# Kernel tuning notes

Measured on AMD Instinct MI355X. Metric: run time of the kernel, lower is better.

Reference implementation:

```python
import jax, jax.numpy as jnp
import numpy as np

# Dims: B batch, T target seq, S source seq (self-attn: S==T), V symmetry-rep dim (D4 -> 8),
# M heads-per-group, K groups (num_heads = M*K = 8), F head_rep dim (TrivialRep -> 1),
# Hqk qk head width, Hv v head width, C feature width per rep component.
B, T, S, V, M, K, F, Hqk, Hv, C = 4, 512, 512, 8, 2, 4, 1, 32, 32, 256


def setup_inputs() -> dict:
    key = jax.random.key(0)
    ks = jax.random.split(key, 6)
    x = jax.random.normal(ks[0], (B, T, V, C), jnp.float32)
    # SymDecompLinear kernels: q has extra out reps (F, M, K); k/v have (F, 1, K) -> m axis broadcast
    Wq = jax.random.normal(ks[1], (C, M, K, F, Hqk), jnp.float32) / np.sqrt(C).astype(np.float32)
    Wk = jax.random.normal(ks[2], (C, K, F, Hqk), jnp.float32) / np.sqrt(C).astype(np.float32)
    Wv = jax.random.normal(ks[3], (C, K, F, Hv), jnp.float32) / np.sqrt(C).astype(np.float32)
    # out projection contracts the (M, K, F, Hv) head structure back to C features
    Wout = jax.random.normal(ks[4], (M, K, F, Hv, C), jnp.float32) / np.sqrt(M * K * F * Hv).astype(np.float32)
    mask = jax.random.bernoulli(ks[5], 0.9, (B, T, S))
    mask = mask.at[..., 0].set(True)  # guarantee each query attends to >=1 key
    return dict(x=x, Wq=Wq, Wk=Wk, Wv=Wv, Wout=Wout, mask=mask)


def reference(x, Wq, Wk, Wv, Wout, mask):
    # projections: q -> [B,T,V,M,K,F,Hqk]; k,v -> [B,S,V,K,F,H] (single head per group, broadcast over m)
    q = jnp.einsum('btvc,cmkfh->btvmkfh', x, Wq)
    k = jnp.einsum('bsvc,ckfh->bsvkfh', x, Wk)
    v = jnp.einsum('bsvc,ckfh->bsvkfh', x, Wv)
    scale = 1.0 / np.sqrt(F * Hqk).astype(np.float32)
    # logits retain the symmetry axis v: [B,T,S,V,M,K]
    logits = scale * jnp.einsum('btvmkfh,bsvkfh->btsvmk', q, k)
    lgmsk = mask[..., :, :, None, None, None]  # [B,T,S,1,1,1]
    weight = jax.nn.softmax(logits, axis=-4, where=lgmsk)  # softmax over source axis s
    att = jnp.einsum('btsvmk,bsvkfh->btvmkfh', weight, v)
    out = jnp.einsum('btvmkfh,mkfhc->btvc', att, Wout)
    return out
```

## Files before the change

kernel.cpp:

```cpp
#include <hip/hip_runtime.h>
#include <hip/hip_bf16.h>
#include <cstdint>

#define BB 4
#define TT 512
#define SS 512
#define VV 8
#define NROWS (BB * TT * VV)

typedef __attribute__((ext_vector_type(8))) short bf16x8;
typedef __attribute__((ext_vector_type(4))) float f32x4;

static __device__ __forceinline__ short f2bf(float f) {
  union { float f; unsigned u; } x; x.f = f;
  unsigned r = x.u + 0x7FFFu + ((x.u >> 16) & 1u);
  return (short)(r >> 16);
}

static __device__ __forceinline__ unsigned cvt_pk(float lo, float hi) {
  unsigned r;
  asm("v_cvt_pk_bf16_f32 %0, %1, %2" : "=v"(r) : "v"(lo), "v"(hi));
  return r;
}

__global__ __launch_bounds__(256) void pack_w_kernel(const float* __restrict__ Wq,
                                                     const float* __restrict__ Wk,
                                                     const float* __restrict__ Wv,
                                                     const float* __restrict__ Wout,
                                                     short* __restrict__ WcatT,
                                                     short* __restrict__ WoutT) {
  int idx = blockIdx.x * 256 + threadIdx.x;
  const float qscale = 0.17677669529663687f * 1.4426950408889634f;
  if (idx < 512 * 256) {
    int n = idx >> 8, c = idx & 255;
    float val;
    if (n < 256)      val = Wq[c * 256 + n] * qscale;
    else if (n < 384) val = Wk[c * 128 + (n - 256)];
    else              val = Wv[c * 128 + (n - 384)];
    WcatT[idx] = f2bf(val);
  } else {
    int j = idx - 512 * 256;
    int cc = j >> 8, jj = j & 255;
    WoutT[j] = f2bf(Wout[jj * 256 + cc]);
  }
}

__global__ __launch_bounds__(256) void pack_mask_kernel(const int* __restrict__ mask,
                                                        unsigned long long* __restrict__ mask64) {
  int row = blockIdx.x * 4 + (threadIdx.x >> 6);
  int ln = threadIdx.x & 63;
  const int* mrow = mask + (size_t)row * SS;
#pragma unroll
  for (int c = 0; c < 8; ++c) {
    unsigned long long bal = __ballot(mrow[c * 64 + ln] != 0);
    if (ln == 0) mask64[(size_t)row * 8 + c] = bal;
  }
}

__global__ __launch_bounds__(256) void vtrans_kernel(const short* __restrict__ qkv,
                                                     short* __restrict__ Vt) {
  const int sc = blockIdx.x;
  const int v = blockIdx.y, b = blockIdx.z;
  const int k = threadIdx.x & 3;
  const int sp = threadIdx.x >> 2;
  const int s = sc * 128 + sp * 2;
  const short* src0 = qkv + ((size_t)((b * TT + s) * VV + v)) * 512 + 384 + k * 32;
  const short* src1 = src0 + VV * 512;
  bf16x8 r0[4], r1[4];
#pragma unroll
  for (int i = 0; i < 4; ++i) {
    r0[i] = *(const bf16x8*)(src0 + i * 8);
    r1[i] = *(const bf16x8*)(src1 + i * 8);
  }
  short* dst = Vt + ((size_t)((b * VV + v) * 4 + k)) * 32 * 512 + s;
#pragma unroll
  for (int h = 0; h < 32; ++h) {
    unsigned pk = (unsigned)(unsigned short)r0[h >> 3][h & 7] |
                  ((unsigned)(unsigned short)r1[h >> 3][h & 7] << 16);
    *(unsigned*)(dst + (size_t)h * 512) = pk;
  }
}

template <int N, bool AF32, bool OUTF32>
__global__ __launch_bounds__(256) void gemm_bf16(const void* __restrict__ Ap,
                                                 const short* __restrict__ Bt,
                                                 void* __restrict__ Cout) {
  __shared__ short As[128][64];
  __shared__ short Bs[128][64];
  const int tid = threadIdx.x;
  const int w = tid >> 6, ln = tid & 63;
  const int wr = (w >> 1) * 64, wc = (w & 1) * 64;
  const int bm = blockIdx.x * 128, bn = blockIdx.y * 128;
  const int lr = ln & 15, lk = (ln >> 4) * 8;
  const int r0 = tid >> 3, ko = (tid & 7) * 8;

  f32x4 acc[4][4] = {};

  for (int k0 = 0; k0 < 256; k0 += 64) {
    bf16x8 a[4], bb[4];
#pragma unroll
    for (int i = 0; i < 4; ++i) {
      size_t row = (size_t)(bm + i * 32 + r0);
      if constexpr (AF32) {
        const float* Af = (const float*)Ap;
        float4 f0 = *(const float4*)&Af[row * 256 + k0 + ko];
        float4 f1 = *(const float4*)&Af[row * 256 + k0 + ko + 4];
        uint4 pk = make_uint4(cvt_pk(f0.x, f0.y), cvt_pk(f0.z, f0.w),
                              cvt_pk(f1.x, f1.y), cvt_pk(f1.z, f1.w));
        a[i] = *(bf16x8*)&pk;
      } else {
        a[i] = *(const bf16x8*)&((const short*)Ap)[row * 256 + k0 + ko];
      }
      bb[i] = *(const bf16x8*)&Bt[(size_t)(bn + i * 32 + r0) * 256 + k0 + ko];
    }
    __syncthreads();
#pragma unroll
    for (int i = 0; i < 4; ++i) {
      *(bf16x8*)&As[i * 32 + r0][ko] = a[i];
      *(bf16x8*)&Bs[i * 32 + r0][ko] = bb[i];
    }
    __syncthreads();

#pragma unroll
    for (int kk = 0; kk < 2; ++kk) {
      bf16x8 af[4], bfr[4];
#pragma unroll
      for (int mi = 0; mi < 4; ++mi)
        af[mi] = *(const bf16x8*)&As[wr + mi * 16 + lr][kk * 32 + lk];
#pragma unroll
      for (int ni = 0; ni < 4; ++ni)
        bfr[ni] = *(const bf16x8*)&Bs[wc + ni * 16 + lr][kk * 32 + lk];
#pragma unroll
      for (int mi = 0; mi < 4; ++mi)
#pragma unroll
        for (int ni = 0; ni < 4; ++ni)
          acc[mi][ni] = __builtin_amdgcn_mfma_f32_16x16x32_bf16(af[mi], bfr[ni], acc[mi][ni], 0, 0, 0);
    }
  }

  const int rowg = (ln >> 4) * 4;
#pragma unroll
  for (int mi = 0; mi < 4; ++mi)
#pragma unroll
    for (int r = 0; r < 4; ++r) {
      size_t row = bm + wr + mi * 16 + rowg + r;
      if constexpr (OUTF32) {
#pragma unroll
        for (int ni = 0; ni < 4; ++ni)
          ((float*)Cout)[row * N + bn + wc + ni * 16 + lr] = acc[mi][ni][r];
      } else {
        unsigned u0 = cvt_pk(acc[mi][0][r], acc[mi][1][r]);
        unsigned u1 = cvt_pk(acc[mi][2][r], acc[mi][3][r]);
        short* Cs = (short*)Cout + row * N + bn + wc + lr;
        Cs[0]  = (short)u0;
        Cs[16] = (short)(u0 >> 16);
        Cs[32] = (short)u1;
        Cs[48] = (short)(u1 >> 16);
      }
    }
}

__global__ __launch_bounds__(256) void attn_mfma(const short* __restrict__ qkv,
                                                 const short* __restrict__ Vt,
                                                 const unsigned long long* __restrict__ mask64,
                                                 short* __restrict__ att) {
  const int t0 = blockIdx.x * 64;
  const int v  = blockIdx.y >> 2;
  const int k  = blockIdx.y & 3;
  const int b  = blockIdx.z;
  const int tid = threadIdx.x;
  const int w  = tid >> 6;
  const int ln = tid & 63;
  const int gq = ln >> 4;
  const int tr = ln & 15;

  __shared__ __align__(16) short Pt[4][16][72];

  bf16x8 qf[2];
  {
    const short* qp = qkv + ((size_t)((b*TT + t0 + w*16 + tr)*VV + v))*512 + k*32 + gq*8;
    qf[0] = *(const bf16x8*)qp;
    qf[1] = *(const bf16x8*)(qp + 128);
  }

  f32x4 acc_o[2][2] = {};
  float l_run[2] = {0.f, 0.f};

  const short* kbase = qkv + ((size_t)(b*TT*VV + v))*512 + 256 + k*32 + gq*8;
  const short* vbase = Vt + ((size_t)((b*VV + v)*4 + k))*32*512 + (size_t)tr*512 + gq*8;
  const unsigned long long* mrow = mask64 + ((size_t)(b*TT + t0 + w*16 + tr))*8;

  bf16x8 kf[4], vf[2][2];
  unsigned long long mb;
#pragma unroll
  for (int st = 0; st < 4; ++st)
    kf[st] = *(const bf16x8*)(kbase + (size_t)(st*16 + tr) * (VV*512));
#pragma unroll
  for (int sh = 0; sh < 2; ++sh)
#pragma unroll
    for (int hh = 0; hh < 2; ++hh)
      vf[sh][hh] = *(const bf16x8*)(vbase + hh*16*512 + sh*32);
  mb = mrow[0];

  for (int c = 0; c < 8; ++c) {
    bf16x8 kn[4], vn[2][2];
    unsigned long long mbn;
    if (c < 7) {
      const int sb = (c + 1) * 64;
#pragma unroll
      for (int st = 0; st < 4; ++st)
        kn[st] = *(const bf16x8*)(kbase + (size_t)(sb + st*16 + tr) * (VV*512));
#pragma unroll
      for (int sh = 0; sh < 2; ++sh)
#pragma unroll
        for (int hh = 0; hh < 2; ++hh)
          vn[sh][hh] = *(const bf16x8*)(vbase + hh*16*512 + sb + sh*32);
      mbn = mrow[c + 1];
    }

    unsigned mlo = (unsigned)mb, mhi = (unsigned)(mb >> 32);
    float bias[4][4];
#pragma unroll
    for (int st = 0; st < 4; ++st) {
      unsigned wbits = (st < 2) ? mlo : mhi;
      const int base = (st & 1) * 16 + 4 * gq;
#pragma unroll
      for (int r = 0; r < 4; ++r)
        bias[st][r] = ((wbits >> (base + r)) & 1u) ? 0.f : -INFINITY;
    }

#pragma unroll
    for (int m = 0; m < 2; ++m) {
      f32x4 lac[4];
#pragma unroll
      for (int st = 0; st < 4; ++st) {
        f32x4 z = {0.f, 0.f, 0.f, 0.f};
        lac[st] = __builtin_amdgcn_mfma_f32_16x16x32_bf16(kf[st], qf[m], z, 0, 0, 0);
      }
      float pl[4][4];
      float rs = 0.f;
#pragma unroll
      for (int st = 0; st < 4; ++st)
#pragma unroll
        for (int r = 0; r < 4; ++r) {
          pl[st][r] = exp2f(lac[st][r] + bias[st][r]);
          rs += pl[st][r];
        }
      rs += __shfl_xor(rs, 16);
      rs += __shfl_xor(rs, 32);
      l_run[m] += rs;

#pragma unroll
      for (int st = 0; st < 4; ++st)
        *(uint2*)&Pt[w][tr][st * 16 + 4 * gq] =
            make_uint2(cvt_pk(pl[st][0], pl[st][1]), cvt_pk(pl[st][2], pl[st][3]));
#pragma unroll
      for (int sh = 0; sh < 2; ++sh) {
        bf16x8 pf = *(const bf16x8*)&Pt[w][tr][sh * 32 + gq * 8];
#pragma unroll
        for (int hh = 0; hh < 2; ++hh)
          acc_o[m][hh] = __builtin_amdgcn_mfma_f32_16x16x32_bf16(pf, vf[sh][hh], acc_o[m][hh], 0, 0, 0);
      }
    }

    if (c < 7) {
#pragma unroll
      for (int st = 0; st < 4; ++st) kf[st] = kn[st];
#pragma unroll
      for (int sh = 0; sh < 2; ++sh)
#pragma unroll
        for (int hh = 0; hh < 2; ++hh) vf[sh][hh] = vn[sh][hh];
      mb = mbn;
    }
  }

#pragma unroll
  for (int m = 0; m < 2; ++m) {
    float invR[4];
#pragma unroll
    for (int r = 0; r < 4; ++r) invR[r] = 1.f / __shfl(l_run[m], 4 * gq + r);
#pragma unroll
    for (int r = 0; r < 4; ++r) {
      short* dst = att + ((size_t)((b*TT + t0 + w*16 + 4*gq + r)*VV + v))*256
                 + m*128 + k*32 + tr;
      unsigned u = cvt_pk(acc_o[m][0][r] * invR[r], acc_o[m][1][r] * invR[r]);
      dst[0]  = (short)u;
      dst[16] = (short)(u >> 16);
    }
  }
}

extern "C" void kernel_launch(void* const* d_in, const int* in_sizes, int n_in,
                              void* d_out, int out_size, void* d_ws, size_t ws_size,
                              hipStream_t stream) {
  const float* x = (const float*)d_in[0];
  const float* Wq = (const float*)d_in[1];
  const float* Wk = (const float*)d_in[2];
  const float* Wv = (const float*)d_in[3];
  const float* Wout = (const float*)d_in[4];
  const int* mask = (const int*)d_in[5];
  float* out = (float*)d_out;

  short* WcatT = (short*)d_ws;
  short* WoutT = WcatT + 512 * 256;
  short* qkv   = WoutT + 256 * 256;
  short* att   = qkv + (size_t)NROWS * 512;
  short* Vt    = att + (size_t)NROWS * 256;
  unsigned long long* mask64 = (unsigned long long*)(Vt + (size_t)128 * 32 * 512);

  pack_w_kernel<<<(512 * 256 + 256 * 256) / 256, 256, 0, stream>>>(Wq, Wk, Wv, Wout, WcatT, WoutT);
  pack_mask_kernel<<<BB * TT / 4, 256, 0, stream>>>(mask, mask64);
  gemm_bf16<512, true, false><<<dim3(NROWS / 128, 4), 256, 0, stream>>>(x, WcatT, qkv);
  vtrans_kernel<<<dim3(4, VV, BB), 256, 0, stream>>>(qkv, Vt);
  attn_mfma<<<dim3(TT / 64, VV * 4, BB), 256, 0, stream>>>(qkv, Vt, mask64, att);
  gemm_bf16<256, false, true><<<dim3(NROWS / 128, 2), 256, 0, stream>>>(att, WoutT, out);
}
```

Before: 75.22 us.

## Store QKV head-major and tile V transpose; merge weight and mask packing kernels

The QKV GEMM epilogue now writes its output in a per-(batch, view, head) contiguous layout, [bv][head][t][32]. K loads in the attention kernel therefore become contiguous 64-byte rows instead of strided by V*512. The V transpose is rewritten to read this layout and to write V^T in 64-column tiles, and the weight packing and mask packing kernels are merged into a single launch. The goal is better memory coalescing in attention and one less kernel launch. In exchange, the GEMM epilogue now does scattered 2-byte stores with more index arithmetic.

Result: faster. 68.55 us (-8.9%).

```diff
diff --git a/kernel.cpp b/kernel.cpp
--- a/kernel.cpp
+++ b/kernel.cpp
@@ -8,6 +8,7 @@
 #define VV 8
 #define NROWS (BB * TT * VV)
 
+
 typedef __attribute__((ext_vector_type(8))) short bf16x8;
 typedef __attribute__((ext_vector_type(4))) float f32x4;
 
@@ -23,65 +24,63 @@
   return r;
 }
 
-__global__ __launch_bounds__(256) void pack_w_kernel(const float* __restrict__ Wq,
-                                                     const float* __restrict__ Wk,
-                                                     const float* __restrict__ Wv,
-                                                     const float* __restrict__ Wout,
-                                                     short* __restrict__ WcatT,
-                                                     short* __restrict__ WoutT) {
-  int idx = blockIdx.x * 256 + threadIdx.x;
-  const float qscale = 0.17677669529663687f * 1.4426950408889634f;
-  if (idx < 512 * 256) {
-    int n = idx >> 8, c = idx & 255;
-    float val;
-    if (n < 256)      val = Wq[c * 256 + n] * qscale;
-    else if (n < 384) val = Wk[c * 128 + (n - 256)];
-    else              val = Wv[c * 128 + (n - 384)];
-    WcatT[idx] = f2bf(val);
+__global__ __launch_bounds__(256) void pack_all_kernel(const float* __restrict__ Wq,
+                                                       const float* __restrict__ Wk,
+                                                       const float* __restrict__ Wv,
+                                                       const float* __restrict__ Wout,
+                                                       const int* __restrict__ mask,
+                                                       short* __restrict__ WcatT,
+                                                       short* __restrict__ WoutT,
+                                                       unsigned long long* __restrict__ mask64) {
+  if (blockIdx.x < 768) {
+    int idx = blockIdx.x * 256 + threadIdx.x;
+    const float qscale = 0.17677669529663687f * 1.4426950408889634f;
+    if (idx < 512 * 256) {
+      int n = idx >> 8, c = idx & 255;
+      float val;
+      if (n < 256)      val = Wq[c * 256 + n] * qscale;
+      else if (n < 384) val = Wk[c * 128 + (n - 256)];
+      else              val = Wv[c * 128 + (n - 384)];
+      WcatT[idx] = f2bf(val);
+    } else {
+      int j = idx - 512 * 256;
+      int cc = j >> 8, jj = j & 255;
+      WoutT[j] = f2bf(Wout[jj * 256 + cc]);
+    }
   } else {
-    int j = idx - 512 * 256;
-    int cc = j >> 8, jj = j & 255;
-    WoutT[j] = f2bf(Wout[jj * 256 + cc]);
-  }
-}
-
-__global__ __launch_bounds__(256) void pack_mask_kernel(const int* __restrict__ mask,
-                                                        unsigned long long* __restrict__ mask64) {
-  int row = blockIdx.x * 4 + (threadIdx.x >> 6);
-  int ln = threadIdx.x & 63;
-  const int* mrow = mask + (size_t)row * SS;
-#pragma unroll
-  for (int c = 0; c < 8; ++c) {
-    unsigned long long bal = __ballot(mrow[c * 64 + ln] != 0);
-    if (ln == 0) mask64[(size_t)row * 8 + c] = bal;
-  }
-}
-
-__global__ __launch_bounds__(256) void vtrans_kernel(const short* __restrict__ qkv,
-                                                     short* __restrict__ Vt) {
-  const int sc = blockIdx.x;
-  const int v = blockIdx.y, b = blockIdx.z;
-  const int k = threadIdx.x & 3;
-  const int sp = threadIdx.x >> 2;
-  const int s = sc * 128 + sp * 2;
-  const short* src0 = qkv + ((size_t)((b * TT + s) * VV + v)) * 512 + 384 + k * 32;
-  const short* src1 = src0 + VV * 512;
+    int row = (blockIdx.x - 768) * 4 + (threadIdx.x >> 6);
+    int ln = threadIdx.x & 63;
+    const int* mrow = mask + (size_t)row * SS;
+#pragma unroll
+    for (int c = 0; c < 8; ++c) {
+      unsigned long long bal = __ballot(mrow[c * 64 + ln] != 0);
+      if (ln == 0) mask64[(size_t)row * 8 + c] = bal;
+    }
+  }
+}
+
+__global__ __launch_bounds__(256) void vtrans_kernel(const short* __restrict__ qkvh,
+                                                     short* __restrict__ Vt2) {
+  const int hd = blockIdx.x;
+  const int bv = hd >> 2, k = hd & 3;
+  const int s0 = threadIdx.x * 2;
+  const short* src = qkvh + ((size_t)(bv * 16 + 12 + k) * 512 + s0) * 32;
   bf16x8 r0[4], r1[4];
 #pragma unroll
   for (int i = 0; i < 4; ++i) {
-    r0[i] = *(const bf16x8*)(src0 + i * 8);
-    r1[i] = *(const bf16x8*)(src1 + i * 8);
-  }
-  short* dst = Vt + ((size_t)((b * VV + v) * 4 + k)) * 32 * 512 + s;
+    r0[i] = *(const bf16x8*)(src + i * 8);
+    r1[i] = *(const bf16x8*)(src + 32 + i * 8);
+  }
+  short* dst = Vt2 + (size_t)hd * 16384 + (s0 >> 6) * 2048 + (s0 & 63);
 #pragma unroll
   for (int h = 0; h < 32; ++h) {
     unsigned pk = (unsigned)(unsigned short)r0[h >> 3][h & 7] |
                   ((unsigned)(unsigned short)r1[h >> 3][h & 7] << 16);
-    *(unsigned*)(dst + (size_t)h * 512) = pk;
-  }
-}
-
-template <int N, bool AF32, bool OUTF32>
+    *(unsigned*)(dst + h * 64) = pk;
+  }
+}
+
+template <int N, bool AF32, int EPI>
 __global__ __launch_bounds__(256) void gemm_bf16(const void* __restrict__ Ap,
                                                  const short* __restrict__ Bt,
                                                  void* __restrict__ Cout) {
@@ -139,29 +138,44 @@
   }
 
   const int rowg = (ln >> 4) * 4;
-#pragma unroll
-  for (int mi = 0; mi < 4; ++mi)
-#pragma unroll
-    for (int r = 0; r < 4; ++r) {
-      size_t row = bm + wr + mi * 16 + rowg + r;
-      if constexpr (OUTF32) {
+  if constexpr (EPI == 0) {
+#pragma unroll
+    for (int mi = 0; mi < 4; ++mi)
+#pragma unroll
+      for (int r = 0; r < 4; ++r) {
+        size_t row = bm + wr + mi * 16 + rowg + r;
 #pragma unroll
         for (int ni = 0; ni < 4; ++ni)
           ((float*)Cout)[row * N + bn + wc + ni * 16 + lr] = acc[mi][ni][r];
-      } else {
+      }
+  } else {
+    int soff[4];
+#pragma unroll
+    for (int ni = 0; ni < 4; ++ni) {
+      int j = bn + wc + ni * 16 + lr;
+      soff[ni] = (j >> 5) * (512 * 32) + (j & 31);
+    }
+    short* q16 = (short*)Cout;
+#pragma unroll
+    for (int mi = 0; mi < 4; ++mi)
+#pragma unroll
+      for (int r = 0; r < 4; ++r) {
+        int row = bm + wr + mi * 16 + rowg + r;
+        int t = (row >> 3) & 511;
+        int bv = (row >> 12) * 8 + (row & 7);
+        size_t base = ((size_t)bv << 18) + (t << 5);
         unsigned u0 = cvt_pk(acc[mi][0][r], acc[mi][1][r]);
         unsigned u1 = cvt_pk(acc[mi][2][r], acc[mi][3][r]);
-        short* Cs = (short*)Cout + row * N + bn + wc + lr;
-        Cs[0]  = (short)u0;
-        Cs[16] = (short)(u0 >> 16);
-        Cs[32] = (short)u1;
-        Cs[48] = (short)(u1 >> 16);
-      }
-    }
-}
-
-__global__ __launch_bounds__(256) void attn_mfma(const short* __restrict__ qkv,
-                                                 const short* __restrict__ Vt,
+        q16[base + soff[0]] = (short)u0;
+        q16[base + soff[1]] = (short)(u0 >> 16);
+        q16[base + soff[2]] = (short)u1;
+        q16[base + soff[3]] = (short)(u1 >> 16);
+      }
+  }
+}
+
+__global__ __launch_bounds__(256) void attn_mfma(const short* __restrict__ qkvh,
+                                                 const short* __restrict__ Vt2,
                                                  const unsigned long long* __restrict__ mask64,
                                                  short* __restrict__ att) {
   const int t0 = blockIdx.x * 64;
@@ -173,48 +187,48 @@
   const int ln = tid & 63;
   const int gq = ln >> 4;
   const int tr = ln & 15;
+  const int bv = b * 8 + v;
 
   __shared__ __align__(16) short Pt[4][16][72];
 
   bf16x8 qf[2];
   {
-    const short* qp = qkv + ((size_t)((b*TT + t0 + w*16 + tr)*VV + v))*512 + k*32 + gq*8;
+    const short* qp = qkvh + ((size_t)(bv * 16 + k) * 512 + (t0 + w * 16 + tr)) * 32 + gq * 8;
     qf[0] = *(const bf16x8*)qp;
-    qf[1] = *(const bf16x8*)(qp + 128);
+    qf[1] = *(const bf16x8*)(qp + 4 * 512 * 32);
   }
 
   f32x4 acc_o[2][2] = {};
   float l_run[2] = {0.f, 0.f};
 
-  const short* kbase = qkv + ((size_t)(b*TT*VV + v))*512 + 256 + k*32 + gq*8;
-  const short* vbase = Vt + ((size_t)((b*VV + v)*4 + k))*32*512 + (size_t)tr*512 + gq*8;
-  const unsigned long long* mrow = mask64 + ((size_t)(b*TT + t0 + w*16 + tr))*8;
+  const short* kb = qkvh + (size_t)(bv * 16 + 8 + k) * 16384 + gq * 8;
+  const short* vb = Vt2 + (size_t)(bv * 4 + k) * 16384 + tr * 64 + gq * 8;
+  const unsigned long long* mrow = mask64 + ((size_t)(b * TT + t0 + w * 16 + tr)) * 8;
 
   bf16x8 kf[4], vf[2][2];
   unsigned long long mb;
 #pragma unroll
   for (int st = 0; st < 4; ++st)
-    kf[st] = *(const bf16x8*)(kbase + (size_t)(st*16 + tr) * (VV*512));
+    kf[st] = *(const bf16x8*)(kb + (size_t)(st * 16 + tr) * 32);
 #pragma unroll
   for (int sh = 0; sh < 2; ++sh)
 #pragma unroll
     for (int hh = 0; hh < 2; ++hh)
-      vf[sh][hh] = *(const bf16x8*)(vbase + hh*16*512 + sh*32);
+      vf[sh][hh] = *(const bf16x8*)(vb + hh * 16 * 64 + sh * 32);
   mb = mrow[0];
 
   for (int c = 0; c < 8; ++c) {
     bf16x8 kn[4], vn[2][2];
     unsigned long long mbn;
     if (c < 7) {
-      const int sb = (c + 1) * 64;
 #pragma unroll
       for (int st = 0; st < 4; ++st)
-        kn[st] = *(const bf16x8*)(kbase + (size_t)(sb + st*16 + tr) * (VV*512));
+        kn[st] = *(const bf16x8*)(kb + (size_t)((c + 1) * 64 + st * 16 + tr) * 32);
 #pragma unroll
       for (int sh = 0; sh < 2; ++sh)
 #pragma unroll
         for (int hh = 0; hh < 2; ++hh)
-          vn[sh][hh] = *(const bf16x8*)(vbase + hh*16*512 + sb + sh*32);
+          vn[sh][hh] = *(const bf16x8*)(vb + (c + 1) * 2048 + hh * 16 * 64 + sh * 32);
       mbn = mrow[c + 1];
     }
 
@@ -281,8 +295,8 @@
     for (int r = 0; r < 4; ++r) invR[r] = 1.f / __shfl(l_run[m], 4 * gq + r);
 #pragma unroll
     for (int r = 0; r < 4; ++r) {
-      short* dst = att + ((size_t)((b*TT + t0 + w*16 + 4*gq + r)*VV + v))*256
-                 + m*128 + k*32 + tr;
+      short* dst = att + ((size_t)((b * TT + t0 + w * 16 + 4 * gq + r) * VV + v)) * 256
+                 + m * 128 + k * 32 + tr;
       unsigned u = cvt_pk(acc_o[m][0][r] * invR[r], acc_o[m][1][r] * invR[r]);
       dst[0]  = (short)u;
       dst[16] = (short)(u >> 16);
@@ -303,15 +317,14 @@
 
   short* WcatT = (short*)d_ws;
   short* WoutT = WcatT + 512 * 256;
-  short* qkv   = WoutT + 256 * 256;
-  short* att   = qkv + (size_t)NROWS * 512;
-  short* Vt    = att + (size_t)NROWS * 256;
-  unsigned long long* mask64 = (unsigned long long*)(Vt + (size_t)128 * 32 * 512);
-
-  pack_w_kernel<<<(512 * 256 + 256 * 256) / 256, 256, 0, stream>>>(Wq, Wk, Wv, Wout, WcatT, WoutT);
-  pack_mask_kernel<<<BB * TT / 4, 256, 0, stream>>>(mask, mask64);
-  gemm_bf16<512, true, false><<<dim3(NROWS / 128, 4), 256, 0, stream>>>(x, WcatT, qkv);
-  vtrans_kernel<<<dim3(4, VV, BB), 256, 0, stream>>>(qkv, Vt);
-  attn_mfma<<<dim3(TT / 64, VV * 4, BB), 256, 0, stream>>>(qkv, Vt, mask64, att);
-  gemm_bf16<256, false, true><<<dim3(NROWS / 128, 2), 256, 0, stream>>>(att, WoutT, out);
-}
+  short* qkvh  = WoutT + 256 * 256;
+  short* att   = qkvh + (size_t)NROWS * 512;
+  short* Vt2   = att + (size_t)NROWS * 256;
+  unsigned long long* mask64 = (unsigned long long*)(Vt2 + (size_t)128 * 16384);
+
+  pack_all_kernel<<<768 + 512, 256, 0, stream>>>(Wq, Wk, Wv, Wout, mask, WcatT, WoutT, mask64);
+  gemm_bf16<512, true, 2><<<dim3(NROWS / 128, 4), 256, 0, stream>>>(x, WcatT, qkvh);
+  vtrans_kernel<<<128, 256, 0, stream>>>(qkvh, Vt2);
+  attn_mfma<<<dim3(TT / 64, VV * 4, BB), 256, 0, stream>>>(qkvh, Vt2, mask64, att);
+  gemm_bf16<256, false, 0><<<dim3(NROWS / 128, 2), 256, 0, stream>>>(att, WoutT, out);
+}
```
